# Kernel tuning notes

Measured on AMD Instinct MI355X. Metric: run time of the kernel, lower is better.

## Reference

```python
import jax, jax.numpy as jnp
import numpy as np

VOCAB, EMBED, HIDDEN = 32000, 100, 128
B, T = 1024, 256


def setup_inputs() -> dict:
    key = jax.random.key(0)
    ks = jax.random.split(key, 8)
    s_e = 1.0 / np.sqrt(HIDDEN)  # torch nn.RNN init scale
    x = jax.random.randint(ks[0], (B, T), 0, VOCAB, dtype=jnp.int64)
    emb = jax.random.normal(ks[1], (VOCAB, EMBED), dtype=jnp.float32)
    W_ih = jax.random.uniform(ks[2], (HIDDEN, EMBED), jnp.float32, -s_e, s_e)
    W_hh = jax.random.uniform(ks[3], (HIDDEN, HIDDEN), jnp.float32, -s_e, s_e)
    b_ih = jax.random.uniform(ks[4], (HIDDEN,), jnp.float32, -s_e, s_e)
    b_hh = jax.random.uniform(ks[5], (HIDDEN,), jnp.float32, -s_e, s_e)
    s_f = 1.0 / np.sqrt(HIDDEN)
    W_fc = jax.random.uniform(ks[6], (VOCAB, HIDDEN), jnp.float32, -s_f, s_f)
    b_fc = jax.random.uniform(ks[7], (VOCAB,), jnp.float32, -s_f, s_f)
    return {"x": x, "emb": emb, "W_ih": W_ih, "W_hh": W_hh,
            "b_ih": b_ih, "b_hh": b_hh, "W_fc": W_fc, "b_fc": b_fc}


def reference(x, emb, W_ih, W_hh, b_ih, b_hh, W_fc, b_fc):
    # embedding lookup: [B,T] -> [B,T,E]
    embedded = emb[x]
    # precompute input projections for all timesteps: [B,T,H]
    xp = jnp.einsum('bte,he->bth', embedded, W_ih) + b_ih + b_hh
    xp_t = jnp.swapaxes(xp, 0, 1)  # [T,B,H]

    def step(h, xt):
        h = jnp.tanh(xt + h @ W_hh.T)
        return h, None

    h0 = jnp.zeros((x.shape[0], W_hh.shape[0]), dtype=emb.dtype)
    h_last, _ = jax.lax.scan(step, h0, xp_t)
    # final-step linear head: [B,H] -> [B,V]
    return h_last @ W_fc.T + b_fc
```

## Files before the change

### kernel.cpp

```cpp
#include <hip/hip_runtime.h>
#include <hip/hip_bf16.h>

#define V_ 32000
#define E_ 100
#define H_ 128
#define B_ 1024
#define T_ 256

typedef float f32x4 __attribute__((ext_vector_type(4)));
typedef int   i32x4 __attribute__((ext_vector_type(4)));
typedef __bf16 bf16x8 __attribute__((ext_vector_type(8)));
typedef __bf16 bf16x4 __attribute__((ext_vector_type(4)));

__device__ __forceinline__ f32x4 mfma16(bf16x8 a, bf16x8 b, f32x4 c) {
    return __builtin_amdgcn_mfma_f32_16x16x32_bf16(a, b, c, 0, 0, 0);
}


__global__ void k0_emb(const float* __restrict__ emb, __bf16* __restrict__ embb) {
    int i = blockIdx.x * 256 + threadIdx.x;
    int e4 = i * 4;
    int v = e4 >> 7, k = e4 & 127;
    if (v >= V_) return;
    bf16x4 o;
    if (k < E_) {
        f32x4 p = *(const f32x4*)&emb[(size_t)v * E_ + k];
#pragma unroll
        for (int r = 0; r < 4; ++r) o[r] = (__bf16)p[r];
    } else {
#pragma unroll
        for (int r = 0; r < 4; ++r) o[r] = (__bf16)0.0f;
    }
    *(bf16x4*)&embb[(size_t)v * 128 + k] = o;
}

__global__ void k0_wih(const float* __restrict__ Wih, __bf16* __restrict__ wihb) {
    int tid = threadIdx.x;
#pragma unroll
    for (int i = 0; i < 4; ++i) {
        int t2 = tid + i * 512;
        int tile = t2 >> 8, row4 = (t2 >> 4) & 15, ch = t2 & 15;
        int grow = tile * 16 + row4;
        int g = tile * 256 + ch * 16 + row4;
        bf16x8 o;
#pragma unroll
        for (int e = 0; e < 8; ++e) {
            int k = ch * 8 + e;
            o[e] = (k < E_) ? (__bf16)Wih[(size_t)grow * E_ + k] : (__bf16)0.0f;
        }
        *(bf16x8*)&wihb[(size_t)g * 8] = o;
    }
}

__global__ __launch_bounds__(512, 1) void k1_xproj(
    const int* __restrict__ x, const __bf16* __restrict__ embb,
    const __bf16* __restrict__ wihb, const float* __restrict__ bih,
    const float* __restrict__ bhh, __bf16* __restrict__ xpb)
{
    const int tid = threadIdx.x;
    const int lane = tid & 63, w = tid >> 6;
    const int nt = w >> 1;
    const int mh = w & 1;
    const int b0 = blockIdx.x * 64;
    const int t0 = blockIdx.y * 4;
    const int sub = lane >> 4, rc = lane & 15;

    bf16x8 af[4][4];
#pragma unroll
    for (int m = 0; m < 4; ++m)
#pragma unroll
        for (int kc = 0; kc < 4; ++kc)
            af[m][kc] = *(const bf16x8*)&wihb[(size_t)(((mh * 4 + m) * 256) + kc * 64 + lane) * 8];

    f32x4 bias4[4];
#pragma unroll
    for (int m = 0; m < 4; ++m) {
        int h0 = (mh * 4 + m) * 16 + sub * 4;
        bias4[m] = *(const f32x4*)&bih[h0] + *(const f32x4*)&bhh[h0];
    }

    i32x4 xr4 = *(const i32x4*)&x[(size_t)(b0 + nt * 16 + rc) * T_ + t0];

#pragma unroll
    for (int tt = 0; tt < 4; ++tt) {
        int xv = xr4[tt];
        bf16x8 bf[4];
#pragma unroll
        for (int kc = 0; kc < 4; ++kc)
            bf[kc] = *(const bf16x8*)&embb[(size_t)xv * 128 + (kc * 4 + sub) * 8];

        f32x4 acc[4];
#pragma unroll
        for (int m = 0; m < 4; ++m) acc[m] = (f32x4){0.f, 0.f, 0.f, 0.f};
#pragma unroll
        for (int kc = 0; kc < 4; ++kc)
#pragma unroll
            for (int m = 0; m < 4; ++m)
                acc[m] = mfma16(af[m][kc], bf[kc], acc[m]);

#pragma unroll
        for (int m = 0; m < 4; ++m) {
            f32x4 v = acc[m] + bias4[m];
            bf16x4 o;
#pragma unroll
            for (int r = 0; r < 4; ++r) o[r] = (__bf16)v[r];
            __bf16* dst = xpb + ((size_t)(t0 + tt) * B_ + b0 + nt * 16 + rc) * H_
                              + (mh * 4 + m) * 16 + sub * 4;
            *(bf16x4*)dst = o;
        }
    }
}

__global__ __launch_bounds__(512, 1) void k2_rnn(
    const __bf16* __restrict__ xpb, const float* __restrict__ Whh,
    __bf16* __restrict__ hg)
{
    __shared__ __align__(16) __bf16 Hg[2][2048];
    const int tid = threadIdx.x;
    const int lane = tid & 63, w = tid >> 6;
    const int bi = blockIdx.x;
    const int b0 = bi * 16;
    const int sub = lane >> 4, c = lane & 15;

    bf16x8 wah[4];
#pragma unroll
    for (int kc = 0; kc < 4; ++kc) {
        const float* src = Whh + (size_t)(w * 16 + c) * H_ + kc * 32 + sub * 8;
        f32x4 p0 = *(const f32x4*)src, p1 = *(const f32x4*)(src + 4);
        bf16x8 h8;
#pragma unroll
        for (int e = 0; e < 4; ++e) {
            h8[e] = (__bf16)p0[e];
            h8[4 + e] = (__bf16)p1[e];
        }
        wah[kc] = h8;
    }

    if (tid < 256) {
        bf16x8 z8;
#pragma unroll
        for (int e = 0; e < 8; ++e) z8[e] = (__bf16)0.0f;
        *(bf16x8*)&Hg[0][tid * 8] = z8;
    }
    __syncthreads();

    const int i0 = w * 16 + sub * 4;
    const __bf16* xq = xpb + (size_t)(b0 + c) * H_ + i0;
    const size_t xstep = (size_t)B_ * H_;

    const int wb = (((w >> 1) * 64 + ((w & 1) * 2 + (sub >> 1)) * 16 + c) << 3)
                 + (sub & 1) * 4;

    bf16x4 h4;

#define K2_STEP(PK, XREG) do {                                              \
        const __bf16* Hp = &Hg[PK][0];                                      \
        bf16x8 hb0 = *(const bf16x8*)(Hp + lane * 8);                       \
        bf16x8 hb1 = *(const bf16x8*)(Hp + 512 + lane * 8);                 \
        bf16x8 hb2 = *(const bf16x8*)(Hp + 1024 + lane * 8);                \
        bf16x8 hb3 = *(const bf16x8*)(Hp + 1536 + lane * 8);                \
        f32x4 xf;                                                           \
        _Pragma("unroll")                                                   \
        for (int r = 0; r < 4; ++r) xf[r] = (float)XREG[r];                 \
        f32x4 zz = {0.f, 0.f, 0.f, 0.f};                                    \
        f32x4 a0 = mfma16(wah[0], hb0, xf);                                 \
        f32x4 a1 = mfma16(wah[1], hb1, zz);                                 \
        a0 = mfma16(wah[2], hb2, a0);                                       \
        a1 = mfma16(wah[3], hb3, a1);                                       \
        f32x4 s = a0 + a1;                                                  \
        _Pragma("unroll")                                                   \
        for (int r = 0; r < 4; ++r) {                                       \
            float e;                                                        \
            asm("v_exp_f32 %0, %1" : "=v"(e) : "v"(s[r] * 2.8853900817779268f)); \
            float ep1 = e + 1.0f;                                           \
            float rcp;                                                      \
            asm("v_rcp_f32 %0, %1" : "=v"(rcp) : "v"(ep1));                 \
            h4[r] = (__bf16)(1.0f - 2.0f * rcp);                            \
        }                                                                   \
        *(bf16x4*)&Hg[(PK) ^ 1][wb] = h4;                                   \
        asm volatile("s_waitcnt lgkmcnt(0)" ::: "memory");                  \
        __builtin_amdgcn_s_barrier();                                       \
        __builtin_amdgcn_sched_barrier(0);                                  \
    } while (0)

    bf16x4 xc0 = *(const bf16x4*)(xq);
    bf16x4 xc1 = *(const bf16x4*)(xq + xstep);
    bf16x4 xc2 = *(const bf16x4*)(xq + 2 * xstep);
    bf16x4 xc3 = *(const bf16x4*)(xq + 3 * xstep);
    xq += 4 * xstep;

    for (int j = 0; j < T_ / 4; ++j) {
        bf16x4 xn0, xn1, xn2, xn3;
        if (j < T_ / 4 - 1) {
            xn0 = *(const bf16x4*)(xq);
            xn1 = *(const bf16x4*)(xq + xstep);
            xn2 = *(const bf16x4*)(xq + 2 * xstep);
            xn3 = *(const bf16x4*)(xq + 3 * xstep);
            xq += 4 * xstep;
        }
        K2_STEP(0, xc0);
        K2_STEP(1, xc1);
        K2_STEP(0, xc2);
        K2_STEP(1, xc3);
        xc0 = xn0; xc1 = xn1; xc2 = xn2; xc3 = xn3;
    }
#undef K2_STEP

    hg[0] = hg[0];
    *(bf16x4*)&hg[(size_t)(bi >> 3) * 16384 + (size_t)(bi & 7) * 2048 + wb] = h4;
}

__global__ __launch_bounds__(512, 1) void k3_head(
    const float* __restrict__ Wfc, const __bf16* __restrict__ hg,
    const float* __restrict__ bfc, float* __restrict__ out)
{
    const int tid = threadIdx.x;
    const int lane = tid & 63, w = tid >> 6;
    const int gv = blockIdx.x;
    const int v0 = gv * 128;
    const int sub = lane >> 4, rc = lane & 15;
    const int mt0 = (w & 3) * 2, nt0 = (w >> 2) * 4;

    bf16x8 af[2][4];
#pragma unroll
    for (int m = 0; m < 2; ++m)
#pragma unroll
        for (int kc = 0; kc < 4; ++kc) {
            int row = v0 + (mt0 + m) * 16 + rc;
            const float* src = Wfc + (size_t)row * H_ + (kc * 4 + sub) * 8;
            f32x4 p0 = *(const f32x4*)src, p1 = *(const f32x4*)(src + 4);
            bf16x8 h8;
#pragma unroll
            for (int e = 0; e < 4; ++e) {
                h8[e] = (__bf16)p0[e];
                h8[4 + e] = (__bf16)p1[e];
            }
            af[m][kc] = h8;
        }

    f32x4 bias4[2];
#pragma unroll
    for (int m = 0; m < 2; ++m)
        bias4[m] = *(const f32x4*)&bfc[v0 + (mt0 + m) * 16 + sub * 4];

    for (int bt = 0; bt < 8; ++bt) {
        const int b0 = bt * 128;
        f32x4 acc[2][4];
#pragma unroll
        for (int m = 0; m < 2; ++m)
#pragma unroll
            for (int n = 0; n < 4; ++n) acc[m][n] = (f32x4){0.f, 0.f, 0.f, 0.f};

#pragma unroll
        for (int kc = 0; kc < 4; ++kc) {
            bf16x8 bf[4];
#pragma unroll
            for (int n = 0; n < 4; ++n)
                bf[n] = *(const bf16x8*)&hg[(size_t)bt * 16384
                          + (size_t)(((nt0 + n) * 256) + kc * 64 + lane) * 8];
#pragma unroll
            for (int n = 0; n < 4; ++n)
#pragma unroll
                for (int m = 0; m < 2; ++m)
                    acc[m][n] = mfma16(af[m][kc], bf[n], acc[m][n]);
        }
#pragma unroll
        for (int n = 0; n < 4; ++n)
#pragma unroll
            for (int m = 0; m < 2; ++m) {
                f32x4 v = acc[m][n] + bias4[m];
                float* dst = out + (size_t)(b0 + (nt0 + n) * 16 + rc) * V_
                                 + v0 + (mt0 + m) * 16 + sub * 4;
                *(f32x4*)dst = v;
            }
    }
}

extern "C" void kernel_launch(void* const* d_in, const int* in_sizes, int n_in,
                              void* d_out, int out_size, void* d_ws, size_t ws_size,
                              hipStream_t stream) {
    const int*   x   = (const int*)d_in[0];
    const float* emb = (const float*)d_in[1];
    const float* Wih = (const float*)d_in[2];
    const float* Whh = (const float*)d_in[3];
    const float* bih = (const float*)d_in[4];
    const float* bhh = (const float*)d_in[5];
    const float* Wfc = (const float*)d_in[6];
    const float* bfc = (const float*)d_in[7];
    float* out = (float*)d_out;

    const size_t SZ_HG   = 262144;
    const size_t SZ_WIHB = 32768;
    const size_t SZ_EMBB = (size_t)V_ * 128 * 2;
    const size_t SZ_XPB  = (size_t)T_ * B_ * H_ * 2;

    char* wsb = (char*)d_ws;
    size_t off = 0;
    auto take = [&](size_t n) -> char* {
        char* p = wsb + off;
        off += (n + 255) & ~(size_t)255;
        return p;
    };
    char* outb = (char*)d_out;
    size_t ooff = 0;
    auto takeOut = [&](size_t n) -> char* {
        char* p = outb + ooff;
        ooff += (n + 255) & ~(size_t)255;
        return p;
    };
    auto fits = [&](size_t n) { return off + n + 256 <= ws_size; };

    __bf16* hgp   = (__bf16*)take(SZ_HG);
    __bf16* wihb  = (__bf16*)take(SZ_WIHB);
    __bf16* embb  = fits(SZ_EMBB) ? (__bf16*)take(SZ_EMBB) : (__bf16*)takeOut(SZ_EMBB);
    __bf16* xpb   = fits(SZ_XPB)  ? (__bf16*)take(SZ_XPB)  : (__bf16*)takeOut(SZ_XPB);

    k0_emb<<<4000, 256, 0, stream>>>(emb, embb);
    k0_wih<<<1, 512, 0, stream>>>(Wih, wihb);

    k1_xproj<<<dim3(16, 64), 512, 0, stream>>>(x, embb, wihb, bih, bhh, xpb);
    k2_rnn<<<dim3(64), 512, 0, stream>>>(xpb, Whh, hgp);
    k3_head<<<dim3(250), 512, 0, stream>>>(Wfc, hgp, bfc, out);
}
```

Before: 165.5 us.

## Precompute per-vocab input projection table and gather it inside the recurrence

Replaces the per-token input projection (B*T GEMM rows written to a large xp buffer) with a per-vocabulary projection table (V x H) computed once, and has the RNN kernel gather rows of that table by token id each step. This removes the embedding conversion kernels and the large intermediate write and read of the T*B*H buffer. The cost is dependent index loads followed by gathers on the RNN kernel's critical path. Those gathers are prefetched two groups ahead to hide the latency.

```diff
diff --git a/kernel.cpp b/kernel.cpp
--- a/kernel.cpp
+++ b/kernel.cpp
@@ -16,104 +16,81 @@
     return __builtin_amdgcn_mfma_f32_16x16x32_bf16(a, b, c, 0, 0, 0);
 }
 
-
-__global__ void k0_emb(const float* __restrict__ emb, __bf16* __restrict__ embb) {
-    int i = blockIdx.x * 256 + threadIdx.x;
-    int e4 = i * 4;
-    int v = e4 >> 7, k = e4 & 127;
-    if (v >= V_) return;
-    bf16x4 o;
-    if (k < E_) {
-        f32x4 p = *(const f32x4*)&emb[(size_t)v * E_ + k];
-#pragma unroll
-        for (int r = 0; r < 4; ++r) o[r] = (__bf16)p[r];
-    } else {
-#pragma unroll
-        for (int r = 0; r < 4; ++r) o[r] = (__bf16)0.0f;
-    }
-    *(bf16x4*)&embb[(size_t)v * 128 + k] = o;
-}
-
-__global__ void k0_wih(const float* __restrict__ Wih, __bf16* __restrict__ wihb) {
-    int tid = threadIdx.x;
-#pragma unroll
-    for (int i = 0; i < 4; ++i) {
-        int t2 = tid + i * 512;
-        int tile = t2 >> 8, row4 = (t2 >> 4) & 15, ch = t2 & 15;
-        int grow = tile * 16 + row4;
-        int g = tile * 256 + ch * 16 + row4;
-        bf16x8 o;
-#pragma unroll
-        for (int e = 0; e < 8; ++e) {
-            int k = ch * 8 + e;
-            o[e] = (k < E_) ? (__bf16)Wih[(size_t)grow * E_ + k] : (__bf16)0.0f;
-        }
-        *(bf16x8*)&wihb[(size_t)g * 8] = o;
-    }
-}
-
-__global__ __launch_bounds__(512, 1) void k1_xproj(
-    const int* __restrict__ x, const __bf16* __restrict__ embb,
-    const __bf16* __restrict__ wihb, const float* __restrict__ bih,
-    const float* __restrict__ bhh, __bf16* __restrict__ xpb)
+__global__ __launch_bounds__(512, 1) void k0_pp(
+    const float* __restrict__ emb, const float* __restrict__ Wih,
+    const float* __restrict__ bih, const float* __restrict__ bhh,
+    __bf16* __restrict__ pp)
 {
     const int tid = threadIdx.x;
     const int lane = tid & 63, w = tid >> 6;
     const int nt = w >> 1;
     const int mh = w & 1;
-    const int b0 = blockIdx.x * 64;
-    const int t0 = blockIdx.y * 4;
+    const int v0 = blockIdx.x * 64;
     const int sub = lane >> 4, rc = lane & 15;
+    const f32x4 z = {0.f, 0.f, 0.f, 0.f};
 
     bf16x8 af[4][4];
 #pragma unroll
     for (int m = 0; m < 4; ++m)
 #pragma unroll
-        for (int kc = 0; kc < 4; ++kc)
-            af[m][kc] = *(const bf16x8*)&wihb[(size_t)(((mh * 4 + m) * 256) + kc * 64 + lane) * 8];
-
-    f32x4 bias4[4];
+        for (int kc = 0; kc < 4; ++kc) {
+            int row = (mh * 4 + m) * 16 + rc;
+            int k0 = kc * 32 + sub * 8;
+            const float* s = Wih + (size_t)row * E_ + k0;
+            f32x4 p0 = (k0 + 4 <= E_) ? *(const f32x4*)s : z;
+            f32x4 p1 = (k0 + 8 <= E_) ? *(const f32x4*)(s + 4) : z;
+            bf16x8 h8;
+#pragma unroll
+            for (int e = 0; e < 4; ++e) {
+                h8[e] = (__bf16)p0[e];
+                h8[4 + e] = (__bf16)p1[e];
+            }
+            af[m][kc] = h8;
+        }
+
+    bf16x8 bf[4];
+#pragma unroll
+    for (int kc = 0; kc < 4; ++kc) {
+        int vrow = v0 + nt * 16 + rc;
+        int k0 = kc * 32 + sub * 8;
+        const float* s = emb + (size_t)vrow * E_ + k0;
+        f32x4 p0 = (k0 + 4 <= E_) ? *(const f32x4*)s : z;
+        f32x4 p1 = (k0 + 8 <= E_) ? *(const f32x4*)(s + 4) : z;
+        bf16x8 h8;
+#pragma unroll
+        for (int e = 0; e < 4; ++e) {
+            h8[e] = (__bf16)p0[e];
+            h8[4 + e] = (__bf16)p1[e];
+        }
+        bf[kc] = h8;
+    }
+
+    f32x4 acc[4];
 #pragma unroll
     for (int m = 0; m < 4; ++m) {
         int h0 = (mh * 4 + m) * 16 + sub * 4;
-        bias4[m] = *(const f32x4*)&bih[h0] + *(const f32x4*)&bhh[h0];
-    }
-
-    i32x4 xr4 = *(const i32x4*)&x[(size_t)(b0 + nt * 16 + rc) * T_ + t0];
-
-#pragma unroll
-    for (int tt = 0; tt < 4; ++tt) {
-        int xv = xr4[tt];
-        bf16x8 bf[4];
-#pragma unroll
-        for (int kc = 0; kc < 4; ++kc)
-            bf[kc] = *(const bf16x8*)&embb[(size_t)xv * 128 + (kc * 4 + sub) * 8];
-
-        f32x4 acc[4];
-#pragma unroll
-        for (int m = 0; m < 4; ++m) acc[m] = (f32x4){0.f, 0.f, 0.f, 0.f};
-#pragma unroll
-        for (int kc = 0; kc < 4; ++kc)
-#pragma unroll
-            for (int m = 0; m < 4; ++m)
-                acc[m] = mfma16(af[m][kc], bf[kc], acc[m]);
-
-#pragma unroll
-        for (int m = 0; m < 4; ++m) {
-            f32x4 v = acc[m] + bias4[m];
-            bf16x4 o;
-#pragma unroll
-            for (int r = 0; r < 4; ++r) o[r] = (__bf16)v[r];
-            __bf16* dst = xpb + ((size_t)(t0 + tt) * B_ + b0 + nt * 16 + rc) * H_
-                              + (mh * 4 + m) * 16 + sub * 4;
-            *(bf16x4*)dst = o;
-        }
+        acc[m] = *(const f32x4*)&bih[h0] + *(const f32x4*)&bhh[h0];
+    }
+#pragma unroll
+    for (int kc = 0; kc < 4; ++kc)
+#pragma unroll
+        for (int m = 0; m < 4; ++m)
+            acc[m] = mfma16(af[m][kc], bf[kc], acc[m]);
+
+#pragma unroll
+    for (int m = 0; m < 4; ++m) {
+        int v = v0 + nt * 16 + rc;
+        int h0 = (mh * 4 + m) * 16 + sub * 4;
+        bf16x4 o;
+#pragma unroll
+        for (int r = 0; r < 4; ++r) o[r] = (__bf16)acc[m][r];
+        *(bf16x4*)&pp[(size_t)v * H_ + h0] = o;
     }
 }
 
 __global__ __launch_bounds__(512, 1) void k2_rnn(
-    const __bf16* __restrict__ xpb, const float* __restrict__ Whh,
-    __bf16* __restrict__ hg)
+    const int* __restrict__ x, const __bf16* __restrict__ pp,
+    const float* __restrict__ Whh, __bf16* __restrict__ hg)
 {
     __shared__ __align__(16) __bf16 Hg[2][2048];
     const int tid = threadIdx.x;
@@ -145,8 +122,8 @@
     __syncthreads();
 
     const int i0 = w * 16 + sub * 4;
-    const __bf16* xq = xpb + (size_t)(b0 + c) * H_ + i0;
-    const size_t xstep = (size_t)B_ * H_;
+    const int* xrow = x + (size_t)(b0 + c) * T_;
+    const __bf16* ppi = pp + i0;
 
     const int wb = (((w >> 1) * 64 + ((w & 1) * 2 + (sub >> 1)) * 16 + c) << 3)
                  + (sub & 1) * 4;
@@ -183,30 +160,33 @@
         __builtin_amdgcn_sched_barrier(0);                                  \
     } while (0)
 
-    bf16x4 xc0 = *(const bf16x4*)(xq);
-    bf16x4 xc1 = *(const bf16x4*)(xq + xstep);
-    bf16x4 xc2 = *(const bf16x4*)(xq + 2 * xstep);
-    bf16x4 xc3 = *(const bf16x4*)(xq + 3 * xstep);
-    xq += 4 * xstep;
+    i32x4 xsA = *(const i32x4*)(xrow);
+    bf16x4 xc0 = *(const bf16x4*)(ppi + (size_t)xsA[0] * H_);
+    bf16x4 xc1 = *(const bf16x4*)(ppi + (size_t)xsA[1] * H_);
+    bf16x4 xc2 = *(const bf16x4*)(ppi + (size_t)xsA[2] * H_);
+    bf16x4 xc3 = *(const bf16x4*)(ppi + (size_t)xsA[3] * H_);
+    xsA = *(const i32x4*)(xrow + 4);
 
     for (int j = 0; j < T_ / 4; ++j) {
         bf16x4 xn0, xn1, xn2, xn3;
+        i32x4 xsB = xsA;
         if (j < T_ / 4 - 1) {
-            xn0 = *(const bf16x4*)(xq);
-            xn1 = *(const bf16x4*)(xq + xstep);
-            xn2 = *(const bf16x4*)(xq + 2 * xstep);
-            xn3 = *(const bf16x4*)(xq + 3 * xstep);
-            xq += 4 * xstep;
-        }
+            xn0 = *(const bf16x4*)(ppi + (size_t)xsA[0] * H_);
+            xn1 = *(const bf16x4*)(ppi + (size_t)xsA[1] * H_);
+            xn2 = *(const bf16x4*)(ppi + (size_t)xsA[2] * H_);
+            xn3 = *(const bf16x4*)(ppi + (size_t)xsA[3] * H_);
+        }
+        if (j < T_ / 4 - 2)
+            xsB = *(const i32x4*)(xrow + 4 * (j + 2));
         K2_STEP(0, xc0);
         K2_STEP(1, xc1);
         K2_STEP(0, xc2);
         K2_STEP(1, xc3);
         xc0 = xn0; xc1 = xn1; xc2 = xn2; xc3 = xn3;
+        xsA = xsB;
     }
 #undef K2_STEP
 
-    hg[0] = hg[0];
     *(bf16x4*)&hg[(size_t)(bi >> 3) * 16384 + (size_t)(bi & 7) * 2048 + wb] = h4;
 }
 
@@ -289,10 +269,8 @@
     const float* bfc = (const float*)d_in[7];
     float* out = (float*)d_out;
 
-    const size_t SZ_HG   = 262144;
-    const size_t SZ_WIHB = 32768;
-    const size_t SZ_EMBB = (size_t)V_ * 128 * 2;
-    const size_t SZ_XPB  = (size_t)T_ * B_ * H_ * 2;
+    const size_t SZ_HG = 262144;
+    const size_t SZ_PP = (size_t)V_ * H_ * 2;
 
     char* wsb = (char*)d_ws;
     size_t off = 0;
@@ -301,24 +279,12 @@
         off += (n + 255) & ~(size_t)255;
         return p;
     };
-    char* outb = (char*)d_out;
-    size_t ooff = 0;
-    auto takeOut = [&](size_t n) -> char* {
-        char* p = outb + ooff;
-        ooff += (n + 255) & ~(size_t)255;
-        return p;
-    };
     auto fits = [&](size_t n) { return off + n + 256 <= ws_size; };
 
-    __bf16* hgp   = (__bf16*)take(SZ_HG);
-    __bf16* wihb  = (__bf16*)take(SZ_WIHB);
-    __bf16* embb  = fits(SZ_EMBB) ? (__bf16*)take(SZ_EMBB) : (__bf16*)takeOut(SZ_EMBB);
-    __bf16* xpb   = fits(SZ_XPB)  ? (__bf16*)take(SZ_XPB)  : (__bf16*)takeOut(SZ_XPB);
-
-    k0_emb<<<4000, 256, 0, stream>>>(emb, embb);
-    k0_wih<<<1, 512, 0, stream>>>(Wih, wihb);
-
-    k1_xproj<<<dim3(16, 64), 512, 0, stream>>>(x, embb, wihb, bih, bhh, xpb);
-    k2_rnn<<<dim3(64), 512, 0, stream>>>(xpb, Whh, hgp);
+    __bf16* hgp = (__bf16*)take(SZ_HG);
+    __bf16* pp = fits(SZ_PP) ? (__bf16*)take(SZ_PP) : (__bf16*)d_out;
+
+    k0_pp<<<dim3(500), 512, 0, stream>>>(emb, Wih, bih, bhh, pp);
+    k2_rnn<<<dim3(64), 512, 0, stream>>>(x, pp, Whh, hgp);
     k3_head<<<dim3(250), 512, 0, stream>>>(Wfc, hgp, bfc, out);
 }
```

After: 151.7 us. 8.3% less time.
